# Kernel optimization log

Measured on AMD Instinct MI355X. Metric: run time of the kernel, lower is better.

The kernel has to match this reference:

```python
import jax, jax.numpy as jnp
import numpy as np

N_EMBD = 1024
N_HEAD = 16
HEAD_DIM = N_EMBD // N_HEAD
BLOCK_SIZE = 2048
ROPE_BASE = 10000.0


def _rope_tables(dim, max_len, base=ROPE_BASE):
    half = dim // 2
    freqs = 1.0 / base ** (jnp.arange(half, dtype=jnp.float32) / half)
    angles = jnp.arange(max_len, dtype=jnp.float32)[:, None] * freqs[None, :]  # (T, half)
    return jnp.cos(angles), jnp.sin(angles)


def _apply_rope(x, cos, sin):
    # x: (B, H, T, D); cos/sin: (T, D//2)
    T = x.shape[2]
    c = cos[:T][None, None]
    s = sin[:T][None, None]
    x1 = x[..., ::2]
    x2 = x[..., 1::2]
    out = jnp.stack([x1 * c - x2 * s, x1 * s + x2 * c], axis=-1)  # (B,H,T,D//2,2)
    return out.reshape(x.shape)


def setup_inputs() -> dict:
    key = jax.random.key(0)
    k1, k2, k3, k4, k5 = jax.random.split(key, 5)
    B, T, C = 2, 2048, N_EMBD
    x = jax.random.normal(k1, (B, T, C), dtype=jnp.float32)
    scale = 1.0 / np.sqrt(C)
    Wqkv = jax.random.normal(k2, (C, 3 * C), dtype=jnp.float32) * scale
    bqkv = jax.random.normal(k3, (3 * C,), dtype=jnp.float32) * 0.01
    Wproj = jax.random.normal(k4, (C, C), dtype=jnp.float32) * scale
    bproj = jax.random.normal(k5, (C,), dtype=jnp.float32) * 0.01
    cos, sin = _rope_tables(HEAD_DIM, BLOCK_SIZE)
    return {"x": x, "Wqkv": Wqkv, "bqkv": bqkv, "Wproj": Wproj, "bproj": bproj,
            "cos": cos, "sin": sin}


def reference(x, Wqkv, bqkv, Wproj, bproj, cos, sin):
    B, T, C = x.shape
    H, D = N_HEAD, HEAD_DIM
    qkv = x @ Wqkv + bqkv  # (B,T,3C)
    q, k, v = jnp.split(qkv, 3, axis=-1)
    # (B,T,C) -> (B,H,T,D)
    q = q.reshape(B, T, H, D).transpose(0, 2, 1, 3)
    k = k.reshape(B, T, H, D).transpose(0, 2, 1, 3)
    v = v.reshape(B, T, H, D).transpose(0, 2, 1, 3)
    q = _apply_rope(q, cos, sin)
    k = _apply_rope(k, cos, sin)
    att = jnp.einsum('bhtd,bhsd->bhts', q, k) * (D ** -0.5)
    causal = jnp.tril(jnp.ones((T, T), dtype=bool))
    att = jnp.where(causal[None, None], att, -jnp.inf)
    att = jax.nn.softmax(att, axis=-1)
    y = jnp.einsum('bhts,bhsd->bhtd', att, v)  # (B,H,T,D)
    y = y.transpose(0, 2, 1, 3).reshape(B, T, C)
    return y @ Wproj + bproj
```

## Files before the change

kernel.cpp:

```cpp
#include <hip/hip_runtime.h>
#include <stdint.h>

typedef short s16x8 __attribute__((ext_vector_type(8)));
typedef float f32x4 __attribute__((ext_vector_type(4)));
typedef unsigned short u16;
typedef unsigned int u32;

__device__ __forceinline__ float bf2f(u16 u) {
  union { u32 i; float f; } v; v.i = ((u32)u) << 16; return v.f;
}
__device__ __forceinline__ u16 f2bf(float f) {
  union { float f; u32 i; } v; v.f = f;
  u32 i = v.i;
  return (u16)((i + 0x7fffu + ((i >> 16) & 1u)) >> 16);
}
__device__ __forceinline__ u16 f2bf_fast(float f) {
  union { float f; u32 i; } v; v.f = f;
  return (u16)((v.i + 0x8000u) >> 16);
}

__device__ __forceinline__ s16x8 load8(const void* p, size_t idx, int isf32) {
  s16x8 r;
  if (isf32) {
    const float* f = (const float*)p + idx;
    f32x4 a = *(const f32x4*)f;
    f32x4 b = *(const f32x4*)(f + 4);
#pragma unroll
    for (int j = 0; j < 4; j++) {
      r[j] = (short)f2bf(a[j]);
      r[4 + j] = (short)f2bf(b[j]);
    }
  } else {
    r = *(const s16x8*)((const u16*)p + idx);
  }
  return r;
}
__device__ __forceinline__ float loadf(const void* p, size_t idx, int isf32) {
  return isf32 ? ((const float*)p)[idx] : bf2f(((const u16*)p)[idx]);
}

__device__ __forceinline__ void cp16(const u16* g, u16* l) {
  __builtin_amdgcn_global_load_lds(
      (const __attribute__((address_space(1))) u32*)g,
      (__attribute__((address_space(3))) u32*)l, 16, 0, 0);
}

__global__ void detect_dtype(const u16* __restrict__ x, int* __restrict__ flags) {
  int cnt = 0;
  for (int i = threadIdx.x; i < 4096; i += 64) {
    int e = (x[i] >> 7) & 0xFF;
    if (e >= 0xF0) cnt++;
  }
  unsigned long long any = __ballot(cnt > 0);
  if (threadIdx.x == 0) {
    flags[0] = (any != 0ull) ? 1 : 0;
    flags[1] = 0;
  }
}

__global__ __launch_bounds__(256) void convert_x(const void* __restrict__ x,
                                                 const int* __restrict__ fp,
                                                 u16* __restrict__ xb) {
  int tid = blockIdx.x * 256 + threadIdx.x;
  int r = tid & 127, kq = (tid >> 7) & 3, kB = (tid >> 9) & 31, mB = tid >> 14;
  size_t src = (size_t)(mB * 128 + r) * 1024 + kB * 32 + kq * 8;
  *(s16x8*)(xb + (size_t)tid * 8) = load8(x, src, *fp);
}

__global__ __launch_bounds__(256) void transposeW2(
    const void* __restrict__ Wqkv, const void* __restrict__ Wproj,
    const int* __restrict__ fp, u16* __restrict__ WqkvT,
    u16* __restrict__ WprojT) {
  __shared__ u32 tile32[32 * 66];
  const int f = *fp;
  const int tid = threadIdx.x;
  const int bx = blockIdx.x;
  const void* W;
  u16* WT;
  int N, nb, qkvSide;
  if (bx < 48) { W = Wqkv; WT = WqkvT; N = 3072; nb = bx * 64; qkvSide = 1; }
  else         { W = Wproj; WT = WprojT; N = 1024; nb = (bx - 48) * 64; qkvSide = 0; }
  const int kb = blockIdx.y * 64;
  {
    int a = tid >> 3, c8 = tid & 7;
    s16x8 r0 = load8(W, (size_t)(kb + 2 * a) * N + nb + c8 * 8, f);
    s16x8 r1 = load8(W, (size_t)(kb + 2 * a + 1) * N + nb + c8 * 8, f);
#pragma unroll
    for (int j = 0; j < 8; j++)
      tile32[a * 66 + c8 * 8 + j] = (u32)(u16)r0[j] | ((u32)(u16)r1[j] << 16);
  }
  __syncthreads();
#pragma unroll
  for (int i = 0; i < 2; i++) {
    int idx = tid + i * 256;
    int n = idx & 63, c8 = idx >> 6;
    s16x8 v;
#pragma unroll
    for (int w = 0; w < 4; w++) {
      u32 pk = tile32[(c8 * 4 + w) * 66 + n];
      v[2 * w] = (short)(u16)(pk & 0xFFFF);
      v[2 * w + 1] = (short)(u16)(pk >> 16);
    }
    int R = nb + n, k = kb + c8 * 8;
    int kB = k >> 5, kq = (k >> 3) & 3;
    size_t off;
    if (qkvSide) {
      int nB = R >> 7, r = R & 127;
      off = ((size_t)(nB * 32 + kB) * 4 + kq) * 1024 + r * 8;
    } else {
      int nB = R >> 6, r = R & 63;
      off = (size_t)(nB * 32 + kB) * 2048 + kq * 512 + r * 8;
    }
    *(s16x8*)(WT + off) = v;
  }
}

__global__ __launch_bounds__(256) void transposeV(const u16* __restrict__ qkv,
                                                  u16* __restrict__ vT) {
  __shared__ u32 tile32[64 * 33];
  const int tid = threadIdx.x;
  const int tb = blockIdx.x * 64, bh = blockIdx.y;
  const int b = bh >> 4, h = bh & 15;
  {
    int a = tid >> 3, c8 = tid & 7;
    const u16* base = qkv + (size_t)(b * 2048 + tb + 2 * a) * 3072 + 2048 + h * 64;
    s16x8 r0 = *(const s16x8*)(base + c8 * 8);
    s16x8 r1 = *(const s16x8*)(base + 3072 + c8 * 8);
#pragma unroll
    for (int j = 0; j < 8; j++)
      tile32[(c8 * 8 + j) * 33 + a] = (u32)(u16)r0[j] | ((u32)(u16)r1[j] << 16);
  }
  __syncthreads();
#pragma unroll
  for (int i = 0; i < 2; i++) {
    int idx = tid + i * 256;
    int d = idx >> 3, c8 = idx & 7;
    s16x8 v;
#pragma unroll
    for (int w = 0; w < 4; w++) {
      u32 pk = tile32[d * 33 + c8 * 4 + w];
      v[2 * w] = (short)(u16)(pk & 0xFFFF);
      v[2 * w + 1] = (short)(u16)(pk >> 16);
    }
    *(s16x8*)(vT + ((size_t)bh * 64 + d) * 2048 + tb + c8 * 8) = v;
  }
}

template <int MB, int NT, int KK, int ATILED, int BK>
__global__ __launch_bounds__(256, 6) void gemm_bt(
    const u16* __restrict__ A, int lda, const u16* __restrict__ Bt,
    const void* __restrict__ bias, const int* __restrict__ fI32,
    void* __restrict__ C, int ropeMode, int outF,
    const void* __restrict__ cost, const void* __restrict__ sint, int N) {
  constexpr int MT = MB / 32;
  constexpr int NTW = NT / 32;
  constexpr int KSUB = BK / 32;
  constexpr int KT = KK / BK;
  constexpr int APW = MB / 64;
  constexpr int BPW = NT / 64;
  __shared__ __attribute__((aligned(16))) u16 As[KSUB * MB * 32];
  __shared__ __attribute__((aligned(16))) u16 Bs[KSUB * NT * 32];
  const int inf32 = *fI32;
  const int tid = threadIdx.x;
  const int wave = tid >> 6, lane = tid & 63, quad = lane >> 4, l16 = lane & 15;
  const int bx = blockIdx.x, by = blockIdx.y;
  const int m0 = by * MB, n0 = bx * NT;
  const int wm = (wave & 1) * (MB / 2), wn = (wave >> 1) * (NT / 2);
  f32x4 acc[MT][NTW];
#pragma unroll
  for (int i = 0; i < MT; i++)
#pragma unroll
    for (int j = 0; j < NTW; j++) acc[i][j] = (f32x4){0.f, 0.f, 0.f, 0.f};

  const u16* aT = nullptr;
  const u16* aP = nullptr;
  int mBv = 0, halfA = 0;
  if constexpr (ATILED == 1) {
    mBv = (MB == 128) ? by : (by >> 1);
    halfA = (MB == 128) ? 0 : (by & 1);
    aT = A + (size_t)mBv * KK * 128 + lane * 8;
  } else if constexpr (ATILED == 2) {
    mBv = by >> 1;
    halfA = by & 1;
    aT = A + lane * 8;
  } else {
    const int lr = lane >> 2, lk = (lane & 3) * 8;
    aP = A + (size_t)(m0 + wave * (MB / 4) + lr) * lda + lk;
  }
  const u16* bT = Bt + (size_t)bx * KK * NT + lane * 8;

  for (int s = 0; s < KT; ++s) {
    __syncthreads();
#pragma unroll
    for (int ks = 0; ks < KSUB; ks++) {
      const int kb32 = s * KSUB + ks;
      if constexpr (ATILED == 1) {
#pragma unroll
        for (int j = 0; j < APW; j++) {
          const int c = wave * APW + j;
          size_t off;
          if constexpr (MB == 128) off = (size_t)kb32 * 4096 + c * 512;
          else                     off = (size_t)kb32 * 4096 + c * 1024 + halfA * 512;
          cp16(aT + off, As + ks * (MB * 32) + c * 512);
        }
      } else if constexpr (ATILED == 2) {
        const int vr = mBv * 128 + kb32 * 4 + wave;
        cp16(aT + (size_t)vr * 3072 + halfA * 512,
             As + ks * (MB * 32) + wave * 512);
      } else {
#pragma unroll
        for (int j = 0; j < APW; j++)
          cp16(aP + kb32 * 32 + (size_t)(16 * j) * lda,
               As + ks * (MB * 32) + wave * (APW * 512) + j * 512);
      }
#pragma unroll
      for (int j = 0; j < BPW; j++) {
        const int c = wave * BPW + j;
        cp16(bT + (size_t)kb32 * (NT * 32) + c * 512,
             Bs + ks * (NT * 32) + c * 512);
      }
    }
    __syncthreads();
#pragma unroll
    for (int ks = 0; ks < KSUB; ks++) {
      s16x8 af[MT], bfr[NTW];
#pragma unroll
      for (int mt = 0; mt < MT; mt++) {
        if constexpr (ATILED != 0)
          af[mt] = *(const s16x8*)(As + ks * (MB * 32) + quad * (MB * 8) +
                                   (wm + mt * 16 + l16) * 8);
        else
          af[mt] = *(const s16x8*)(As + ks * (MB * 32) +
                                   (wm + mt * 16 + l16) * 32 + quad * 8);
      }
#pragma unroll
      for (int nt = 0; nt < NTW; nt++)
        bfr[nt] = *(const s16x8*)(Bs + ks * (NT * 32) + quad * (NT * 8) +
                                  (wn + nt * 16 + l16) * 8);
#pragma unroll
      for (int mt = 0; mt < MT; mt++)
#pragma unroll
        for (int nt = 0; nt < NTW; nt++)
          acc[mt][nt] = __builtin_amdgcn_mfma_f32_16x16x32_bf16(
              af[mt], bfr[nt], acc[mt][nt], 0, 0, 0);
    }
  }

#pragma unroll
  for (int nt = 0; nt < NTW; nt++) {
    int col = n0 + wn + nt * 16 + l16;
    float bv = loadf(bias, col, inf32);
    if (ropeMode && col < 2048) {
      int j = (col & 63) >> 1, odd = col & 1;
#pragma unroll
      for (int mt = 0; mt < MT; mt++)
#pragma unroll
        for (int r = 0; r < 4; r++) {
          int row = m0 + wm + mt * 16 + quad * 4 + r, t = row & 2047;
          float cv = loadf(cost, (size_t)t * 32 + j, inf32);
          float sv = loadf(sint, (size_t)t * 32 + j, inf32);
          float val = acc[mt][nt][r] + bv;
          float pr = __shfl_xor(val, 1);
          float res = odd ? (pr * sv + val * cv) : (val * cv - pr * sv);
          ((u16*)C)[(size_t)row * N + col] = f2bf(res);
        }
    } else if (outF && inf32) {
#pragma unroll
      for (int mt = 0; mt < MT; mt++)
#pragma unroll
        for (int r = 0; r < 4; r++) {
          int row = m0 + wm + mt * 16 + quad * 4 + r;
          ((float*)C)[(size_t)row * N + col] = acc[mt][nt][r] + bv;
        }
    } else {
#pragma unroll
      for (int mt = 0; mt < MT; mt++)
#pragma unroll
        for (int r = 0; r < 4; r++) {
          int row = m0 + wm + mt * 16 + quad * 4 + r;
          ((u16*)C)[(size_t)row * N + col] = f2bf(acc[mt][nt][r] + bv);
        }
    }
  }
}

__device__ __forceinline__ int kvIdx(int chunk, int row) {
  return chunk * 512 + (((row & 56) | ((row ^ chunk) & 7)) << 3);
}
__device__ __forceinline__ int pIdx(int chunk, int row) {
  return chunk * 128 + (((row & 8) | ((row ^ chunk) & 7)) << 3);
}

__global__ __launch_bounds__(512) void attn_kernel(u16* qkv,
                                                   const u16* __restrict__ vT) {
  __shared__ __attribute__((aligned(16))) u16 Ks[8 * 512];
  __shared__ __attribute__((aligned(16))) u16 Vt[8 * 512];
  __shared__ __attribute__((aligned(16))) u16 Pl[8][8 * 128];
  const int tid = threadIdx.x;
  const int wave = tid >> 6, lane = tid & 63, quad = lane >> 4, l16 = lane & 15;
  const int cu = blockIdx.x & 255, round = blockIdx.x >> 8;
  const int p = cu >> 5, bh = cu & 31;
  const int qt = round ? p : 15 - p;
  const int h = bh & 15;
  const size_t rb = (size_t)(bh >> 4) * 2048;
  const int qb = qt * 128;
  const float SCALE = 0.18033688011112042f;

  s16x8 qa0, qa1;
  {
    const u16* qp = qkv + (rb + qb + wave * 16 + l16) * 3072 + h * 64;
    qa0 = *(const s16x8*)(qp + quad * 8);
    qa1 = *(const s16x8*)(qp + 32 + quad * 8);
  }

  f32x4 o[4];
  float l_r[4] = {0.f, 0.f, 0.f, 0.f};
#pragma unroll
  for (int i = 0; i < 4; i++) o[i] = (f32x4){0.f, 0.f, 0.f, 0.f};

  const int nchunks = 2 * qt + 2;
  const int srow = tid >> 3, sc8 = tid & 7;
  const int stIdx = kvIdx(sc8, srow);
  s16x8 kr, vr;
  {
    kr = *(const s16x8*)(qkv + (rb + srow) * 3072 + 1024 + h * 64 + sc8 * 8);
    vr = *(const s16x8*)(vT + ((size_t)bh * 64 + srow) * 2048 + sc8 * 8);
  }

  for (int c = 0; c < nchunks; c++) {
    const int sb = c * 64;
    __syncthreads();
    *(s16x8*)(Ks + stIdx) = kr;
    *(s16x8*)(Vt + stIdx) = vr;
    __syncthreads();
    if (c + 1 < nchunks) {
      const int nb = sb + 64;
      kr = *(const s16x8*)(qkv + (rb + nb + srow) * 3072 + 1024 + h * 64 +
                           sc8 * 8);
      vr = *(const s16x8*)(vT + ((size_t)bh * 64 + srow) * 2048 + nb + sc8 * 8);
    }

    if (sb > qb + wave * 16 + 15) continue;

    f32x4 S[4];
#pragma unroll
    for (int kf = 0; kf < 4; kf++) {
      s16x8 k0 = *(const s16x8*)(Ks + kvIdx(quad, kf * 16 + l16));
      s16x8 k1 = *(const s16x8*)(Ks + kvIdx(quad + 4, kf * 16 + l16));
      f32x4 a = (f32x4){0.f, 0.f, 0.f, 0.f};
      a = __builtin_amdgcn_mfma_f32_16x16x32_bf16(qa0, k0, a, 0, 0, 0);
      a = __builtin_amdgcn_mfma_f32_16x16x32_bf16(qa1, k1, a, 0, 0, 0);
      S[kf] = a;
    }

    u16* P = Pl[wave];
    const int mq = qb + wave * 16;
    const bool needMask = (sb + 63) > mq;
#pragma unroll
    for (int r = 0; r < 4; r++) {
      const int qi = mq + quad * 4 + r;
#pragma unroll
      for (int kf = 0; kf < 4; kf++) {
        float pv = __builtin_amdgcn_exp2f(S[kf][r] * SCALE);
        if (needMask) pv = ((sb + kf * 16 + l16) <= qi) ? pv : 0.f;
        l_r[r] += pv;
        P[pIdx(kf * 2 + (l16 >> 3), quad * 4 + r) + (l16 & 7)] = f2bf_fast(pv);
      }
    }
    asm volatile("s_waitcnt lgkmcnt(0)" ::: "memory");
    s16x8 pa0 = *(const s16x8*)(P + pIdx(quad, l16));
    s16x8 pa1 = *(const s16x8*)(P + pIdx(quad + 4, l16));

#pragma unroll
    for (int dt = 0; dt < 4; dt++) {
      s16x8 vb0 = *(const s16x8*)(Vt + kvIdx(quad, dt * 16 + l16));
      s16x8 vb1 = *(const s16x8*)(Vt + kvIdx(quad + 4, dt * 16 + l16));
      o[dt] = __builtin_amdgcn_mfma_f32_16x16x32_bf16(pa0, vb0, o[dt], 0, 0, 0);
      o[dt] = __builtin_amdgcn_mfma_f32_16x16x32_bf16(pa1, vb1, o[dt], 0, 0, 0);
    }
  }

  float inv[4];
#pragma unroll
  for (int r = 0; r < 4; r++) {
    float rs = l_r[r];
#pragma unroll
    for (int off = 8; off; off >>= 1) rs += __shfl_xor(rs, off);
    inv[r] = 1.0f / fmaxf(rs, 1e-30f);
  }
#pragma unroll
  for (int dt = 0; dt < 4; dt++)
#pragma unroll
    for (int r = 0; r < 4; r++) {
      const int grow = (int)rb + qb + wave * 16 + quad * 4 + r;
      const int col = h * 64 + dt * 16 + l16;
      const int vrow = (grow >> 7) * 128 + (col >> 5) * 4 + ((col >> 3) & 3);
      qkv[(size_t)vrow * 3072 + 2048 + (grow & 127) * 8 + (col & 7)] =
          f2bf(o[dt][r] * inv[r]);
    }
}

extern "C" void kernel_launch(void* const* d_in, const int* in_sizes, int n_in,
                              void* d_out, int out_size, void* d_ws,
                              size_t ws_size, hipStream_t stream) {
  const void* x = d_in[0];
  const void* Wqkv = d_in[1];
  const void* bqkv = d_in[2];
  const void* Wproj = d_in[3];
  const void* bproj = d_in[4];
  const void* cost = d_in[5];
  const void* sint = d_in[6];

  int* flags = (int*)d_ws;
  u16* WqkvT = (u16*)d_ws + 128;
  u16* WprojT = WqkvT + (size_t)3072 * 1024;
  u16* qkv = WprojT + (size_t)1024 * 1024;
  u16* yb = qkv + 2048;
  u16* xb = (u16*)d_out;
  u16* vT = (u16*)d_out + (size_t)4096 * 1024;

  detect_dtype<<<1, 64, 0, stream>>>((const u16*)x, flags);
  convert_x<<<2048, 256, 0, stream>>>(x, flags, xb);
  transposeW2<<<dim3(64, 16), 256, 0, stream>>>(Wqkv, Wproj, flags, WqkvT,
                                                WprojT);
  gemm_bt<64, 128, 1024, 1, 64><<<dim3(24, 64), 256, 0, stream>>>(
      xb, 1024, WqkvT, bqkv, flags, qkv, 1, 0, cost, sint, 3072);
  transposeV<<<dim3(32, 32), 256, 0, stream>>>(qkv, vT);
  attn_kernel<<<512, 512, 0, stream>>>(qkv, vT);
  gemm_bt<64, 64, 1024, 2, 64><<<dim3(16, 64), 256, 0, stream>>>(
      yb, 3072, WprojT, bproj, flags, d_out, 0, 1, nullptr, nullptr, 1024);
}
```

Measured before the change: 198.1 us.

## Fuse V transpose into QKV GEMM epilogue and stage attention output via LDS

Removes the separate transposeV kernel. The QKV GEMM blocks that produce V columns now transpose their tile through shared memory and write V^T directly, instead of storing V and re-reading it. The attention kernel's output is also staged through the Ks/Vt shared buffers so it can be written back to the qkv buffer as 16-byte vector stores rather than scattered 2-byte stores. This saves one launch and one round trip of V through global memory, at the cost of extra syncthreads and shared-memory traffic in both epilogues.

```diff
diff --git a/kernel.cpp b/kernel.cpp
--- a/kernel.cpp
+++ b/kernel.cpp
@@ -115,51 +115,22 @@
   }
 }
 
-__global__ __launch_bounds__(256) void transposeV(const u16* __restrict__ qkv,
-                                                  u16* __restrict__ vT) {
-  __shared__ u32 tile32[64 * 33];
-  const int tid = threadIdx.x;
-  const int tb = blockIdx.x * 64, bh = blockIdx.y;
-  const int b = bh >> 4, h = bh & 15;
-  {
-    int a = tid >> 3, c8 = tid & 7;
-    const u16* base = qkv + (size_t)(b * 2048 + tb + 2 * a) * 3072 + 2048 + h * 64;
-    s16x8 r0 = *(const s16x8*)(base + c8 * 8);
-    s16x8 r1 = *(const s16x8*)(base + 3072 + c8 * 8);
-#pragma unroll
-    for (int j = 0; j < 8; j++)
-      tile32[(c8 * 8 + j) * 33 + a] = (u32)(u16)r0[j] | ((u32)(u16)r1[j] << 16);
-  }
-  __syncthreads();
-#pragma unroll
-  for (int i = 0; i < 2; i++) {
-    int idx = tid + i * 256;
-    int d = idx >> 3, c8 = idx & 7;
-    s16x8 v;
-#pragma unroll
-    for (int w = 0; w < 4; w++) {
-      u32 pk = tile32[d * 33 + c8 * 4 + w];
-      v[2 * w] = (short)(u16)(pk & 0xFFFF);
-      v[2 * w + 1] = (short)(u16)(pk >> 16);
-    }
-    *(s16x8*)(vT + ((size_t)bh * 64 + d) * 2048 + tb + c8 * 8) = v;
-  }
-}
-
 template <int MB, int NT, int KK, int ATILED, int BK>
 __global__ __launch_bounds__(256, 6) void gemm_bt(
     const u16* __restrict__ A, int lda, const u16* __restrict__ Bt,
     const void* __restrict__ bias, const int* __restrict__ fI32,
     void* __restrict__ C, int ropeMode, int outF,
-    const void* __restrict__ cost, const void* __restrict__ sint, int N) {
+    const void* __restrict__ cost, const void* __restrict__ sint, int N,
+    u16* __restrict__ vout) {
   constexpr int MT = MB / 32;
   constexpr int NTW = NT / 32;
   constexpr int KSUB = BK / 32;
   constexpr int KT = KK / BK;
   constexpr int APW = MB / 64;
   constexpr int BPW = NT / 64;
-  __shared__ __attribute__((aligned(16))) u16 As[KSUB * MB * 32];
-  __shared__ __attribute__((aligned(16))) u16 Bs[KSUB * NT * 32];
+  __shared__ __attribute__((aligned(16))) u16 sh[KSUB * (MB + NT) * 32];
+  u16* As = sh;
+  u16* Bs = sh + KSUB * MB * 32;
   const int inf32 = *fI32;
   const int tid = threadIdx.x;
   const int wave = tid >> 6, lane = tid & 63, quad = lane >> 4, l16 = lane & 15;
@@ -246,6 +217,33 @@
     }
   }
 
+  if (ropeMode && n0 >= 2048) {
+    __syncthreads();
+    u16* T = sh;
+#pragma unroll
+    for (int nt = 0; nt < NTW; nt++) {
+      const int colL = wn + nt * 16 + l16;
+      float bv = loadf(bias, n0 + colL, inf32);
+#pragma unroll
+      for (int mt = 0; mt < MT; mt++)
+#pragma unroll
+        for (int r = 0; r < 4; r++)
+          T[colL * 72 + wm + mt * 16 + quad * 4 + r] =
+              f2bf(acc[mt][nt][r] + bv);
+    }
+    __syncthreads();
+    const int b = m0 >> 11, t0 = m0 & 2047, h0 = (n0 - 2048) >> 6;
+    const int hd = tid >> 1, seg = tid & 1;
+    const int h = h0 + (hd >> 6), d = hd & 63;
+    u16* dst = vout + ((size_t)((b * 16 + h) * 64 + d)) * 2048 + t0 + seg * 32;
+    const u16* src = T + hd * 72 + seg * 32;
+    *(s16x8*)(dst) = *(const s16x8*)(src);
+    *(s16x8*)(dst + 8) = *(const s16x8*)(src + 8);
+    *(s16x8*)(dst + 16) = *(const s16x8*)(src + 16);
+    *(s16x8*)(dst + 24) = *(const s16x8*)(src + 24);
+    return;
+  }
+
 #pragma unroll
   for (int nt = 0; nt < NTW; nt++) {
     int col = n0 + wn + nt * 16 + l16;
@@ -388,16 +386,27 @@
     for (int off = 8; off; off >>= 1) rs += __shfl_xor(rs, off);
     inv[r] = 1.0f / fmaxf(rs, 1e-30f);
   }
-#pragma unroll
-  for (int dt = 0; dt < 4; dt++)
+
+  __syncthreads();
+#pragma unroll
+  for (int dt = 0; dt < 4; dt++) {
+    u16* base = (dt < 2) ? Ks : Vt;
+    const int gl = (dt & 1) * 2 + (l16 >> 3);
 #pragma unroll
     for (int r = 0; r < 4; r++) {
-      const int grow = (int)rb + qb + wave * 16 + quad * 4 + r;
-      const int col = h * 64 + dt * 16 + l16;
-      const int vrow = (grow >> 7) * 128 + (col >> 5) * 4 + ((col >> 3) & 3);
-      qkv[(size_t)vrow * 3072 + 2048 + (grow & 127) * 8 + (col & 7)] =
-          f2bf(o[dt][r] * inv[r]);
-    }
+      const int rowL = wave * 16 + quad * 4 + r;
+      base[gl * 1024 + rowL * 8 + (l16 & 7)] = f2bf(o[dt][r] * inv[r]);
+    }
+  }
+  __syncthreads();
+  {
+    const int g = tid >> 6, part = tid & 63;
+    const u16* src = (g < 4 ? Ks + g * 1024 : Vt + (g - 4) * 1024) + part * 16;
+    const int vrow = ((int)(rb >> 7) + qt) * 128 + h * 8 + g;
+    u16* dst = qkv + (size_t)vrow * 3072 + 2048 + part * 16;
+    *(s16x8*)(dst) = *(const s16x8*)(src);
+    *(s16x8*)(dst + 8) = *(const s16x8*)(src + 8);
+  }
 }
 
 extern "C" void kernel_launch(void* const* d_in, const int* in_sizes, int n_in,
@@ -424,9 +433,9 @@
   transposeW2<<<dim3(64, 16), 256, 0, stream>>>(Wqkv, Wproj, flags, WqkvT,
                                                 WprojT);
   gemm_bt<64, 128, 1024, 1, 64><<<dim3(24, 64), 256, 0, stream>>>(
-      xb, 1024, WqkvT, bqkv, flags, qkv, 1, 0, cost, sint, 3072);
-  transposeV<<<dim3(32, 32), 256, 0, stream>>>(qkv, vT);
+      xb, 1024, WqkvT, bqkv, flags, qkv, 1, 0, cost, sint, 3072, vT);
   attn_kernel<<<512, 512, 0, stream>>>(qkv, vT);
   gemm_bt<64, 64, 1024, 2, 64><<<dim3(16, 64), 256, 0, stream>>>(
-      yb, 3072, WprojT, bproj, flags, d_out, 0, 1, nullptr, nullptr, 1024);
-}
+      yb, 3072, WprojT, bproj, flags, d_out, 0, 1, nullptr, nullptr, 1024,
+      nullptr);
+}
```

Result: no change. 198.7 us (+0.3%).
